# Performance work log

Hardware: AMD Instinct MI355X
Metric: run time of the kernel (lower is better)

## Reference

```python
import jax, jax.numpy as jnp
import numpy as np

NUM_HEADS = 8
LN_EPS = 1e-6


def _layer_norm(x, gamma, beta):
    mu = jnp.mean(x, axis=-1, keepdims=True)
    var = jnp.mean(jnp.square(x - mu), axis=-1, keepdims=True)
    return (x - mu) / jnp.sqrt(var + LN_EPS) * gamma + beta


def setup_inputs() -> dict:
    key = jax.random.key(0)
    B, S, H, F = 4, 2048, 1024, 4096
    ks = jax.random.split(key, 12)
    scale = 1.0 / np.sqrt(H)
    x = jax.random.normal(ks[0], (B, S, H), dtype=jnp.float32)
    # additive padding mask: 1 where masked, 0 where attended
    mask = jax.random.randint(ks[1], (B, 1, 1, S), 0, 2).astype(jnp.float32)
    Wq = jax.random.normal(ks[2], (H, H), dtype=jnp.float32) * scale
    Wk = jax.random.normal(ks[3], (H, H), dtype=jnp.float32) * scale
    Wv = jax.random.normal(ks[4], (H, H), dtype=jnp.float32) * scale
    Wo = jax.random.normal(ks[5], (H, H), dtype=jnp.float32) * scale
    W1 = jax.random.normal(ks[6], (H, F), dtype=jnp.float32) * scale
    b1 = jnp.zeros((F,), dtype=jnp.float32)
    W2 = jax.random.normal(ks[7], (F, H), dtype=jnp.float32) * (1.0 / np.sqrt(F))
    b2 = jnp.zeros((H,), dtype=jnp.float32)
    gamma = jnp.ones((H,), dtype=jnp.float32)
    beta = jnp.zeros((H,), dtype=jnp.float32)
    return {"x": x, "mask": mask, "Wq": Wq, "Wk": Wk, "Wv": Wv, "Wo": Wo,
            "W1": W1, "b1": b1, "W2": W2, "b2": b2, "gamma": gamma, "beta": beta}


def reference(x, mask, Wq, Wk, Wv, Wo, W1, b1, W2, b2, gamma, beta):
    B, S, H = x.shape
    nh = NUM_HEADS
    d = H // nh

    def split_heads(t):
        return t.reshape(B, S, nh, d).transpose(0, 2, 1, 3)  # [B,nh,S,d]

    q = split_heads(x @ Wq)
    k = split_heads(x @ Wk)
    v = split_heads(x @ Wv)

    # FAITHFUL to source bug: score /= d**(-0.5)  ==  score * sqrt(d)
    scores = jnp.einsum('bhqd,bhkd->bhqk', q, k) * jnp.sqrt(jnp.float32(d))
    scores = scores + mask * (-1e9)
    attn = jax.nn.softmax(scores, axis=-1)
    ctx = jnp.einsum('bhqk,bhkd->bhqd', attn, v)
    ctx = ctx.transpose(0, 2, 1, 3).reshape(B, S, H)
    attn_out = ctx @ Wo

    # dropout = identity (eval mode)
    x = _layer_norm(x + attn_out, gamma, beta)
    ffn = jnp.maximum(x @ W1 + b1, 0.0) @ W2 + b2
    x = _layer_norm(x + ffn, gamma, beta)
    return x
```

## Files before the change

### kernel.cpp

```cpp
#include <hip/hip_runtime.h>


typedef __bf16 bf16;
typedef __bf16 bf16x4 __attribute__((ext_vector_type(4)));
typedef __bf16 bf16x8 __attribute__((ext_vector_type(8)));
typedef float  f32x4  __attribute__((ext_vector_type(4)));

#define MFMA16(a, b, c) __builtin_amdgcn_mfma_f32_16x16x32_bf16(a, b, c, 0, 0, 0)

typedef const __attribute__((address_space(1))) void* gas_cptr;
typedef __attribute__((address_space(3))) void* las_ptr;

__device__ __forceinline__ void g2l16(const void* g, void* l) {
    __builtin_amdgcn_global_load_lds((gas_cptr)g, (las_ptr)l, 16, 0, 0);
}

__device__ __forceinline__ uint b16bits(bf16 v) {
    union { bf16 h; unsigned short u; } cv; cv.h = v; return (uint)cv.u;
}

__global__ __launch_bounds__(256) void split_f32_k(
    const float* __restrict__ in, bf16* __restrict__ hi, bf16* __restrict__ lo)
{
    const long i = (long)blockIdx.x * 256 + threadIdx.x;
    const float4 v = *(const float4*)(in + i * 4);
    const float a[4] = {v.x, v.y, v.z, v.w};
    bf16x4 h, l;
#pragma unroll
    for (int j = 0; j < 4; j++) {
        h[j] = (bf16)a[j];
        l[j] = (bf16)(a[j] - (float)h[j]);
    }
    *(bf16x4*)(hi + i * 4) = h;
    *(bf16x4*)(lo + i * 4) = l;
}

__global__ __launch_bounds__(256) void transpose_f32_k(
    const float* __restrict__ in, bf16* __restrict__ out_hi, bf16* __restrict__ out_lo,
    int in_rs, int out_rs)
{
    __shared__ uint Th[64][33];
    __shared__ uint Tl[64][33];
    const long c0 = (long)blockIdx.x * 64;
    const long r0 = (long)blockIdx.y * 64;
    const int t = threadIdx.x, rp = t >> 3, cc = t & 7;
    const float* pa = in + (r0 + 2 * rp) * (long)in_rs + c0 + cc * 8;
    const float* pb = pa + in_rs;
    float a[8], b[8];
    *(float4*)&a[0] = *(const float4*)pa;
    *(float4*)&a[4] = *(const float4*)(pa + 4);
    *(float4*)&b[0] = *(const float4*)pb;
    *(float4*)&b[4] = *(const float4*)(pb + 4);
#pragma unroll
    for (int j = 0; j < 8; j++) {
        const bf16 ah = (bf16)a[j], bh = (bf16)b[j];
        Th[cc * 8 + j][rp] = b16bits(ah) | (b16bits(bh) << 16);
        const bf16 al = (bf16)(a[j] - (float)ah), bl = (bf16)(b[j] - (float)bh);
        Tl[cc * 8 + j][rp] = b16bits(al) | (b16bits(bl) << 16);
    }
    __syncthreads();
#pragma unroll
    for (int i = 0; i < 2; i++) {
        const int task = i * 256 + t;
        const int c = task >> 3, ch = task & 7;
        uint4 wv;
        wv.x = Th[c][ch * 4 + 0]; wv.y = Th[c][ch * 4 + 1];
        wv.z = Th[c][ch * 4 + 2]; wv.w = Th[c][ch * 4 + 3];
        *(uint4*)(out_hi + (c0 + c) * (long)out_rs + r0 + ch * 8) = wv;
        if (out_lo) {
            uint4 wl;
            wl.x = Tl[c][ch * 4 + 0]; wl.y = Tl[c][ch * 4 + 1];
            wl.z = Tl[c][ch * 4 + 2]; wl.w = Tl[c][ch * 4 + 3];
            *(uint4*)(out_lo + (c0 + c) * (long)out_rs + r0 + ch * 8) = wl;
        }
    }
}

__global__ __launch_bounds__(256) void transpose_bf16_k(
    const bf16* __restrict__ in, bf16* __restrict__ out,
    int in_rs, int out_rs, int nh, long bo_in, long bi_in, long bo_out)
{
    __shared__ uint T[64][33];
    const int z = blockIdx.z;
    const bf16* inp = in + (long)(z / nh) * bo_in + (long)(z % nh) * bi_in;
    bf16* outp = out + (long)z * bo_out;
    const long c0 = (long)blockIdx.x * 64;
    const long r0 = (long)blockIdx.y * 64;
    const int t = threadIdx.x, rp = t >> 3, cc = t & 7;

    const uint4 ra = *(const uint4*)(inp + (r0 + 2 * rp) * (long)in_rs + c0 + cc * 8);
    const uint4 rb = *(const uint4*)(inp + (r0 + 2 * rp + 1) * (long)in_rs + c0 + cc * 8);
    const uint a32[4] = {ra.x, ra.y, ra.z, ra.w};
    const uint b32[4] = {rb.x, rb.y, rb.z, rb.w};
#pragma unroll
    for (int j = 0; j < 8; j++) {
        const uint av = (j & 1) ? (a32[j >> 1] >> 16) : (a32[j >> 1] & 0xffffu);
        const uint bv = (j & 1) ? (b32[j >> 1] >> 16) : (b32[j >> 1] & 0xffffu);
        T[cc * 8 + j][rp] = av | (bv << 16);
    }
    __syncthreads();
#pragma unroll
    for (int i = 0; i < 2; i++) {
        const int task = i * 256 + t;
        const int c = task >> 3, ch = task & 7;
        uint4 wv;
        wv.x = T[c][ch * 4 + 0]; wv.y = T[c][ch * 4 + 1];
        wv.z = T[c][ch * 4 + 2]; wv.w = T[c][ch * 4 + 3];
        *(uint4*)(outp + (c0 + c) * (long)out_rs + r0 + ch * 8) = wv;
    }
}

__global__ __launch_bounds__(256) void gemm_bf16_k(
    const bf16* __restrict__ A, const bf16* __restrict__ Bt,
    bf16* __restrict__ out,
    const float* __restrict__ bias, int relu, int M, int N, int K)
{
    __shared__ __align__(16) bf16 As[128 * 32];
    __shared__ __align__(16) bf16 Bs[128 * 32];
    const int t = threadIdx.x;
    const int fr = t & 15, fq = (t >> 4) & 3;
    const int w = t >> 6, wm = w & 1, wn = w >> 1;
    const long mBase = (long)blockIdx.y * 128;
    const long nBase = (long)blockIdx.x * 128;

    f32x4 acc[4][4];
#pragma unroll
    for (int i = 0; i < 4; i++)
#pragma unroll
        for (int j = 0; j < 4; j++) acc[i][j] = (f32x4){0.f, 0.f, 0.f, 0.f};

    const int arow = t >> 2;
    const int akc  = (t & 3) * 8;
    const bf16* ga0 = A + (mBase + arow) * (long)K + akc;
    const bf16* ga1 = A + (mBase + arow + 64) * (long)K + akc;
    const bf16* gb0 = Bt + (nBase + arow) * (long)K + akc;
    const bf16* gb1 = Bt + (nBase + arow + 64) * (long)K + akc;
    bf16* la0 = &As[t * 8];
    bf16* la1 = &As[(256 + t) * 8];
    bf16* lb0 = &Bs[t * 8];
    bf16* lb1 = &Bs[(256 + t) * 8];

    const int aoff = (wm * 64 + fr) * 32 + fq * 8;
    const int boff = (wn * 64 + fr) * 32 + fq * 8;

    for (int kt = 0; kt < K; kt += 32) {
        g2l16(ga0 + kt, la0);
        g2l16(ga1 + kt, la1);
        g2l16(gb0 + kt, lb0);
        g2l16(gb1 + kt, lb1);
        __syncthreads();
        bf16x8 af[4], bfv[4];
#pragma unroll
        for (int mt = 0; mt < 4; mt++) af[mt] = *(const bf16x8*)&As[aoff + mt * 512];
#pragma unroll
        for (int nt = 0; nt < 4; nt++) bfv[nt] = *(const bf16x8*)&Bs[boff + nt * 512];
#pragma unroll
        for (int mt = 0; mt < 4; mt++)
#pragma unroll
            for (int nt = 0; nt < 4; nt++)
                acc[mt][nt] = MFMA16(af[mt], bfv[nt], acc[mt][nt]);
        __syncthreads();
    }

    const long crow0 = mBase + wm * 64;
    const long ccol0 = nBase + wn * 64;
#pragma unroll
    for (int nt = 0; nt < 4; nt++) {
        const long col = ccol0 + nt * 16 + fr;
        const float bv = bias ? bias[col] : 0.0f;
#pragma unroll
        for (int mt = 0; mt < 4; mt++)
#pragma unroll
            for (int r = 0; r < 4; r++) {
                const long rowg = crow0 + mt * 16 + fq * 4 + r;
                float v = acc[mt][nt][r] + bv;
                if (relu) v = fmaxf(v, 0.0f);
                out[rowg * (long)N + col] = (bf16)v;
            }
    }
}

__global__ __launch_bounds__(256) void gemm_split_k(
    const bf16* __restrict__ Ah, const bf16* __restrict__ Al,
    const bf16* __restrict__ Bh, const bf16* __restrict__ Bl,
    bf16* __restrict__ out_hi, bf16* __restrict__ out_lo, int M, int N, int K)
{
    __shared__ __align__(16) bf16 Ahs[128 * 32];
    __shared__ __align__(16) bf16 Als[128 * 32];
    __shared__ __align__(16) bf16 Bhs[128 * 32];
    __shared__ __align__(16) bf16 Bls[128 * 32];
    const int t = threadIdx.x;
    const int fr = t & 15, fq = (t >> 4) & 3;
    const int w = t >> 6, wm = w & 1, wn = w >> 1;
    const long mBase = (long)blockIdx.y * 128;
    const long nBase = (long)blockIdx.x * 128;

    f32x4 acc[4][4];
#pragma unroll
    for (int i = 0; i < 4; i++)
#pragma unroll
        for (int j = 0; j < 4; j++) acc[i][j] = (f32x4){0.f, 0.f, 0.f, 0.f};

    const int arow = t >> 2;
    const int akc  = (t & 3) * 8;
    const long ga0 = (mBase + arow) * (long)K + akc;
    const long ga1 = (mBase + arow + 64) * (long)K + akc;
    const long gb0 = (nBase + arow) * (long)K + akc;
    const long gb1 = (nBase + arow + 64) * (long)K + akc;

    const int aoff = (wm * 64 + fr) * 32 + fq * 8;
    const int boff = (wn * 64 + fr) * 32 + fq * 8;

    for (int kt = 0; kt < K; kt += 32) {
        g2l16(Ah + ga0 + kt, &Ahs[t * 8]);
        g2l16(Ah + ga1 + kt, &Ahs[(256 + t) * 8]);
        g2l16(Al + ga0 + kt, &Als[t * 8]);
        g2l16(Al + ga1 + kt, &Als[(256 + t) * 8]);
        g2l16(Bh + gb0 + kt, &Bhs[t * 8]);
        g2l16(Bh + gb1 + kt, &Bhs[(256 + t) * 8]);
        g2l16(Bl + gb0 + kt, &Bls[t * 8]);
        g2l16(Bl + gb1 + kt, &Bls[(256 + t) * 8]);
        __syncthreads();
        bf16x8 ah[4], al[4], bh[4], bl[4];
#pragma unroll
        for (int mt = 0; mt < 4; mt++) {
            ah[mt] = *(const bf16x8*)&Ahs[aoff + mt * 512];
            al[mt] = *(const bf16x8*)&Als[aoff + mt * 512];
        }
#pragma unroll
        for (int nt = 0; nt < 4; nt++) {
            bh[nt] = *(const bf16x8*)&Bhs[boff + nt * 512];
            bl[nt] = *(const bf16x8*)&Bls[boff + nt * 512];
        }
#pragma unroll
        for (int mt = 0; mt < 4; mt++)
#pragma unroll
            for (int nt = 0; nt < 4; nt++) {
                acc[mt][nt] = MFMA16(ah[mt], bh[nt], acc[mt][nt]);
                acc[mt][nt] = MFMA16(ah[mt], bl[nt], acc[mt][nt]);
                acc[mt][nt] = MFMA16(al[mt], bh[nt], acc[mt][nt]);
            }
        __syncthreads();
    }

    const long crow0 = mBase + wm * 64;
    const long ccol0 = nBase + wn * 64;
#pragma unroll
    for (int nt = 0; nt < 4; nt++) {
        const long col = ccol0 + nt * 16 + fr;
#pragma unroll
        for (int mt = 0; mt < 4; mt++)
#pragma unroll
            for (int r = 0; r < 4; r++) {
                const long rowg = crow0 + mt * 16 + fq * 4 + r;
                const float v = acc[mt][nt][r];
                const long idx = rowg * (long)N + col;
                const bf16 h = (bf16)v;
                out_hi[idx] = h;
                out_lo[idx] = (bf16)(v - (float)h);
            }
    }
}

#define KROW 136
#define VROW 72
#define PROW 72
__global__ __launch_bounds__(256, 2) void flash_attn_k(
    const bf16* __restrict__ qhi, const bf16* __restrict__ qlo,
    const bf16* __restrict__ khi, const bf16* __restrict__ klo,
    const bf16* __restrict__ vt, const float* __restrict__ mask,
    bf16* __restrict__ ctx)
{
    __shared__ __align__(16) bf16 Kh[64 * KROW];
    __shared__ __align__(16) bf16 Kl[64 * KROW];
    __shared__ __align__(16) bf16 Vs[128 * VROW];
    __shared__ __align__(16) bf16 Ps[4][16 * PROW];
    const float scale = 11.3137085f;
    const int t = threadIdx.x, w = t >> 6;
    const int fr = t & 15, fq = (t >> 4) & 3;
    const int blk = blockIdx.x;
    const int qt = blk & 15, bh_ = blk >> 4, b = bh_ >> 3, h = bh_ & 7;
    const int qrow0 = qt * 128 + w * 16;

    bf16x8 qh[2][4], ql[2][4];
#pragma unroll
    for (int mt = 0; mt < 2; mt++) {
        const long qoff = ((long)(b * 2048 + qrow0 + mt * 64 + fr)) * 1024 + h * 128 + fq * 8;
#pragma unroll
        for (int s = 0; s < 4; s++) {
            qh[mt][s] = *(const bf16x8*)(qhi + qoff + s * 32);
            ql[mt][s] = *(const bf16x8*)(qlo + qoff + s * 32);
        }
    }
    f32x4 o[2][8];
#pragma unroll
    for (int mt = 0; mt < 2; mt++)
#pragma unroll
        for (int nt = 0; nt < 8; nt++) o[mt][nt] = (f32x4){0.f, 0.f, 0.f, 0.f};
    float m_run[2][4], l_run[2][4];
#pragma unroll
    for (int mt = 0; mt < 2; mt++)
#pragma unroll
        for (int r = 0; r < 4; r++) { m_run[mt][r] = -1e30f; l_run[mt][r] = 0.f; }

    const long kbase = (long)(b * 2048) * 1024 + h * 128 + (long)(t & 15) * 8;
    const long vbase = ((long)bh_ * 128) * 2048 + (long)(t & 7) * 8;
    const float* maskb = mask + b * 2048;

    for (int kt = 0; kt < 32; kt++) {
        __syncthreads();
#pragma unroll
        for (int i = 0; i < 4; i++) {
            const int key = i * 16 + (t >> 4);
            const long g = kbase + (long)(kt * 64 + key) * 1024;
            const bf16x8 vk_h = *(const bf16x8*)(khi + g);
            const bf16x8 vk_l = *(const bf16x8*)(klo + g);
            const int d = i * 32 + (t >> 3);
            const bf16x8 vv = *(const bf16x8*)(vt + vbase + (long)d * 2048 + kt * 64);
            *(bf16x8*)&Kh[key * KROW + (t & 15) * 8] = vk_h;
            *(bf16x8*)&Kl[key * KROW + (t & 15) * 8] = vk_l;
            *(bf16x8*)&Vs[d * VROW + (t & 7) * 8] = vv;
        }
        float madd[4];
#pragma unroll
        for (int ct = 0; ct < 4; ct++)
            madd[ct] = maskb[kt * 64 + ct * 16 + fr] * (-1e9f);
        __syncthreads();

        f32x4 sc[2][4];
#pragma unroll
        for (int mt = 0; mt < 2; mt++)
#pragma unroll
            for (int ct = 0; ct < 4; ct++) sc[mt][ct] = (f32x4){0.f, 0.f, 0.f, 0.f};
#pragma unroll
        for (int ct = 0; ct < 4; ct++)
#pragma unroll
            for (int s = 0; s < 4; s++) {
                const int off = (ct * 16 + fr) * KROW + s * 32 + fq * 8;
                const bf16x8 kh8 = *(const bf16x8*)&Kh[off];
                const bf16x8 kl8 = *(const bf16x8*)&Kl[off];
#pragma unroll
                for (int mt = 0; mt < 2; mt++) {
                    sc[mt][ct] = MFMA16(qh[mt][s], kh8, sc[mt][ct]);
                    sc[mt][ct] = MFMA16(qh[mt][s], kl8, sc[mt][ct]);
                    sc[mt][ct] = MFMA16(ql[mt][s], kh8, sc[mt][ct]);
                }
            }

#pragma unroll
        for (int mt = 0; mt < 2; mt++) {
            float alpha[4];
#pragma unroll
            for (int r = 0; r < 4; r++) {
                float mx = sc[mt][0][r] * scale + madd[0];
                mx = fmaxf(mx, sc[mt][1][r] * scale + madd[1]);
                mx = fmaxf(mx, sc[mt][2][r] * scale + madd[2]);
                mx = fmaxf(mx, sc[mt][3][r] * scale + madd[3]);
                mx = fmaxf(mx, __shfl_xor(mx, 1));
                mx = fmaxf(mx, __shfl_xor(mx, 2));
                mx = fmaxf(mx, __shfl_xor(mx, 4));
                mx = fmaxf(mx, __shfl_xor(mx, 8));
                const float mn = fmaxf(m_run[mt][r], mx);
                alpha[r] = __expf(m_run[mt][r] - mn);
                m_run[mt][r] = mn;
            }
            float lt[4] = {0.f, 0.f, 0.f, 0.f};
#pragma unroll
            for (int ct = 0; ct < 4; ct++)
#pragma unroll
                for (int r = 0; r < 4; r++) {
                    const float p = __expf(sc[mt][ct][r] * scale + madd[ct] - m_run[mt][r]);
                    lt[r] += p;
                    Ps[w][(fq * 4 + r) * PROW + ct * 16 + fr] = (bf16)p;
                }
#pragma unroll
            for (int r = 0; r < 4; r++) {
                float s_ = lt[r];
                s_ += __shfl_xor(s_, 1); s_ += __shfl_xor(s_, 2);
                s_ += __shfl_xor(s_, 4); s_ += __shfl_xor(s_, 8);
                l_run[mt][r] = l_run[mt][r] * alpha[r] + s_;
            }
#pragma unroll
            for (int nt = 0; nt < 8; nt++)
#pragma unroll
                for (int r = 0; r < 4; r++) o[mt][nt][r] *= alpha[r];

#pragma unroll
            for (int sp = 0; sp < 2; sp++) {
                const bf16x8 pf = *(const bf16x8*)&Ps[w][fr * PROW + sp * 32 + fq * 8];
#pragma unroll
                for (int nt = 0; nt < 8; nt++) {
                    const bf16x8 vf = *(const bf16x8*)&Vs[(nt * 16 + fr) * VROW + sp * 32 + fq * 8];
                    o[mt][nt] = MFMA16(pf, vf, o[mt][nt]);
                }
            }
        }
    }
#pragma unroll
    for (int mt = 0; mt < 2; mt++)
#pragma unroll
        for (int r = 0; r < 4; r++) {
            const float inv = l_run[mt][r] > 0.f ? 1.0f / l_run[mt][r] : 0.f;
#pragma unroll
            for (int nt = 0; nt < 8; nt++) {
                const long idx = ((long)(b * 2048 + qrow0 + mt * 64 + fq * 4 + r)) * 1024
                               + h * 128 + nt * 16 + fr;
                ctx[idx] = (bf16)(o[mt][nt][r] * inv);
            }
        }
}

__global__ __launch_bounds__(256) void add_ln_k(
    const float* __restrict__ xf, const bf16* __restrict__ y,
    const float* __restrict__ gamma, const float* __restrict__ beta,
    float* __restrict__ out, bf16* __restrict__ out_b)
{
    __shared__ float red[8];
    const long row = blockIdx.x;
    const int t = threadIdx.x, lane = t & 63, w = t >> 6;
    float v[4];
    const float4 xv = *(const float4*)(xf + row * 1024 + t * 4);
    v[0] = xv.x; v[1] = xv.y; v[2] = xv.z; v[3] = xv.w;
    const bf16x4 yv = *(const bf16x4*)(y + row * 1024 + t * 4);
    float s = 0.f, s2 = 0.f;
#pragma unroll
    for (int i = 0; i < 4; i++) {
        v[i] += (float)yv[i];
        s += v[i]; s2 += v[i] * v[i];
    }
#pragma unroll
    for (int off = 1; off < 64; off <<= 1) {
        s += __shfl_xor(s, off);
        s2 += __shfl_xor(s2, off);
    }
    if (lane == 0) { red[w] = s; red[4 + w] = s2; }
    __syncthreads();
    s = red[0] + red[1] + red[2] + red[3];
    s2 = red[4] + red[5] + red[6] + red[7];
    const float mean = s * (1.0f / 1024.0f);
    const float var = s2 * (1.0f / 1024.0f) - mean * mean;
    const float rstd = rsqrtf(var + 1e-6f);
    float4 ov;
    ov.x = (v[0] - mean) * rstd * gamma[t * 4 + 0] + beta[t * 4 + 0];
    ov.y = (v[1] - mean) * rstd * gamma[t * 4 + 1] + beta[t * 4 + 1];
    ov.z = (v[2] - mean) * rstd * gamma[t * 4 + 2] + beta[t * 4 + 2];
    ov.w = (v[3] - mean) * rstd * gamma[t * 4 + 3] + beta[t * 4 + 3];
    *(float4*)(out + row * 1024 + t * 4) = ov;
    if (out_b) {
        bf16x4 hb;
        hb[0] = (bf16)ov.x; hb[1] = (bf16)ov.y; hb[2] = (bf16)ov.z; hb[3] = (bf16)ov.w;
        *(bf16x4*)(out_b + row * 1024 + t * 4) = hb;
    }
}

extern "C" void kernel_launch(void* const* d_in, const int* in_sizes, int n_in,
                              void* d_out, int out_size, void* d_ws, size_t ws_size,
                              hipStream_t stream)
{
    (void)in_sizes; (void)n_in; (void)out_size; (void)ws_size;
    const float* x     = (const float*)d_in[0];
    const float* mask  = (const float*)d_in[1];
    const float* Wq    = (const float*)d_in[2];
    const float* Wk    = (const float*)d_in[3];
    const float* Wv    = (const float*)d_in[4];
    const float* Wo    = (const float*)d_in[5];
    const float* W1    = (const float*)d_in[6];
    const float* b1    = (const float*)d_in[7];
    const float* W2    = (const float*)d_in[8];
    const float* b2    = (const float*)d_in[9];
    const float* gamma = (const float*)d_in[10];
    const float* beta  = (const float*)d_in[11];
    float* out = (float*)d_out;

    char* ws = (char*)d_ws;
    const size_t SZ = 8192ul * 1024 * 2;
    bf16* qhi  = (bf16*)(ws + 0 * SZ);
    bf16* qlo  = (bf16*)(ws + 1 * SZ);
    bf16* khi  = (bf16*)(ws + 2 * SZ);
    bf16* klo  = (bf16*)(ws + 3 * SZ);
    bf16* hbuf = (bf16*)(ws + 0 * SZ);
    bf16* vbuf = (bf16*)(ws + 4 * SZ);
    bf16* ctxb = vbuf;
    bf16* vtb  = (bf16*)(ws + 5 * SZ);
    bf16* fbuf = vtb;
    bf16* xh   = (bf16*)(ws + 6 * SZ);
    bf16* xl   = (bf16*)(ws + 7 * SZ);
    bf16* aob  = xl;
    float* x1f = (float*)(ws + 8 * SZ);
    bf16* x1b  = (bf16*)(ws + 10 * SZ);
    char* wts  = ws + 11 * SZ;
    bf16* Wqth = (bf16*)(wts);
    bf16* Wqtl = (bf16*)(wts + 1 * 2097152);
    bf16* Wkth = (bf16*)(wts + 2 * 2097152);
    bf16* Wktl = (bf16*)(wts + 3 * 2097152);
    bf16* Wvt  = (bf16*)(wts + 4 * 2097152);
    bf16* Wot  = (bf16*)(wts + 5 * 2097152);
    bf16* W1t  = (bf16*)(wts + 6 * 2097152);
    bf16* W2t  = (bf16*)(wts + 6 * 2097152 + 8388608);

    const dim3 blk(256);
    split_f32_k<<<dim3(8192), blk, 0, stream>>>(x, xh, xl);
    transpose_f32_k<<<dim3(16, 16), blk, 0, stream>>>(Wq, Wqth, Wqtl, 1024, 1024);
    transpose_f32_k<<<dim3(16, 16), blk, 0, stream>>>(Wk, Wkth, Wktl, 1024, 1024);
    transpose_f32_k<<<dim3(16, 16), blk, 0, stream>>>(Wv, Wvt, nullptr, 1024, 1024);
    transpose_f32_k<<<dim3(16, 16), blk, 0, stream>>>(Wo, Wot, nullptr, 1024, 1024);
    transpose_f32_k<<<dim3(64, 16), blk, 0, stream>>>(W1, W1t, nullptr, 4096, 1024);
    transpose_f32_k<<<dim3(16, 64), blk, 0, stream>>>(W2, W2t, nullptr, 1024, 4096);
    gemm_split_k<<<dim3(8, 64), blk, 0, stream>>>(xh, xl, Wqth, Wqtl, qhi, qlo, 8192, 1024, 1024);
    gemm_split_k<<<dim3(8, 64), blk, 0, stream>>>(xh, xl, Wkth, Wktl, khi, klo, 8192, 1024, 1024);
    gemm_bf16_k<<<dim3(8, 64), blk, 0, stream>>>(xh, Wvt, vbuf, nullptr, 0, 8192, 1024, 1024);
    transpose_bf16_k<<<dim3(2, 32, 32), blk, 0, stream>>>(vbuf, vtb, 1024, 2048, 8,
                                                          (long)2048 * 1024, 128L, (long)128 * 2048);
    flash_attn_k<<<dim3(512), blk, 0, stream>>>(qhi, qlo, khi, klo, vtb, mask, ctxb);
    gemm_bf16_k<<<dim3(8, 64), blk, 0, stream>>>(ctxb, Wot, aob, nullptr, 0, 8192, 1024, 1024);
    add_ln_k<<<dim3(8192), blk, 0, stream>>>(x, aob, gamma, beta, x1f, x1b);
    gemm_bf16_k<<<dim3(32, 64), blk, 0, stream>>>(x1b, W1t, hbuf, b1, 1, 8192, 4096, 1024);
    gemm_bf16_k<<<dim3(8, 64), blk, 0, stream>>>(hbuf, W2t, fbuf, b2, 0, 8192, 1024, 4096);
    add_ln_k<<<dim3(8192), blk, 0, stream>>>(x1f, fbuf, gamma, beta, out, nullptr);
}
```

Measured before the change: 745.5 us.

## Use 8 waves per flash-attention block with one 16-row tile each

The flash attention kernel now launches 512 threads per block, and each of the 8 waves owns a single 16-row query tile instead of two. This halves per-thread register state and should allow more waves per CU while sharing the same K/V tile. It also wraps the MFMA sections in s_setprio and skips rescaling the output accumulator when no row maximum changed. The risks are heavier barrier synchronisation across more waves and fewer key/value loads per thread to hide latency.

```diff
diff --git a/kernel.cpp b/kernel.cpp
--- a/kernel.cpp
+++ b/kernel.cpp
@@ -265,7 +265,7 @@
 #define KROW 136
 #define VROW 72
 #define PROW 72
-__global__ __launch_bounds__(256, 2) void flash_attn_k(
+__global__ __launch_bounds__(512, 4) void flash_attn_k(
     const bf16* __restrict__ qhi, const bf16* __restrict__ qlo,
     const bf16* __restrict__ khi, const bf16* __restrict__ klo,
     const bf16* __restrict__ vt, const float* __restrict__ mask,
@@ -274,7 +274,7 @@
     __shared__ __align__(16) bf16 Kh[64 * KROW];
     __shared__ __align__(16) bf16 Kl[64 * KROW];
     __shared__ __align__(16) bf16 Vs[128 * VROW];
-    __shared__ __align__(16) bf16 Ps[4][16 * PROW];
+    __shared__ __align__(16) bf16 Ps[8][16 * PROW];
     const float scale = 11.3137085f;
     const int t = threadIdx.x, w = t >> 6;
     const int fr = t & 15, fq = (t >> 4) & 3;
@@ -282,26 +282,21 @@
     const int qt = blk & 15, bh_ = blk >> 4, b = bh_ >> 3, h = bh_ & 7;
     const int qrow0 = qt * 128 + w * 16;
 
-    bf16x8 qh[2][4], ql[2][4];
-#pragma unroll
-    for (int mt = 0; mt < 2; mt++) {
-        const long qoff = ((long)(b * 2048 + qrow0 + mt * 64 + fr)) * 1024 + h * 128 + fq * 8;
+    bf16x8 qh[4], ql[4];
+    {
+        const long qoff = ((long)(b * 2048 + qrow0 + fr)) * 1024 + h * 128 + fq * 8;
 #pragma unroll
         for (int s = 0; s < 4; s++) {
-            qh[mt][s] = *(const bf16x8*)(qhi + qoff + s * 32);
-            ql[mt][s] = *(const bf16x8*)(qlo + qoff + s * 32);
-        }
-    }
-    f32x4 o[2][8];
-#pragma unroll
-    for (int mt = 0; mt < 2; mt++)
-#pragma unroll
-        for (int nt = 0; nt < 8; nt++) o[mt][nt] = (f32x4){0.f, 0.f, 0.f, 0.f};
-    float m_run[2][4], l_run[2][4];
-#pragma unroll
-    for (int mt = 0; mt < 2; mt++)
-#pragma unroll
-        for (int r = 0; r < 4; r++) { m_run[mt][r] = -1e30f; l_run[mt][r] = 0.f; }
+            qh[s] = *(const bf16x8*)(qhi + qoff + s * 32);
+            ql[s] = *(const bf16x8*)(qlo + qoff + s * 32);
+        }
+    }
+    f32x4 o[8];
+#pragma unroll
+    for (int nt = 0; nt < 8; nt++) o[nt] = (f32x4){0.f, 0.f, 0.f, 0.f};
+    float m_run[4], l_run[4];
+#pragma unroll
+    for (int r = 0; r < 4; r++) { m_run[r] = -1e30f; l_run[r] = 0.f; }
 
     const long kbase = (long)(b * 2048) * 1024 + h * 128 + (long)(t & 15) * 8;
     const long vbase = ((long)bh_ * 128) * 2048 + (long)(t & 7) * 8;
@@ -310,12 +305,12 @@
     for (int kt = 0; kt < 32; kt++) {
         __syncthreads();
 #pragma unroll
-        for (int i = 0; i < 4; i++) {
-            const int key = i * 16 + (t >> 4);
+        for (int i = 0; i < 2; i++) {
+            const int key = i * 32 + (t >> 4);
             const long g = kbase + (long)(kt * 64 + key) * 1024;
             const bf16x8 vk_h = *(const bf16x8*)(khi + g);
             const bf16x8 vk_l = *(const bf16x8*)(klo + g);
-            const int d = i * 32 + (t >> 3);
+            const int d = i * 64 + (t >> 3);
             const bf16x8 vv = *(const bf16x8*)(vt + vbase + (long)d * 2048 + kt * 64);
             *(bf16x8*)&Kh[key * KROW + (t & 15) * 8] = vk_h;
             *(bf16x8*)&Kl[key * KROW + (t & 15) * 8] = vk_l;
@@ -327,87 +322,85 @@
             madd[ct] = maskb[kt * 64 + ct * 16 + fr] * (-1e9f);
         __syncthreads();
 
-        f32x4 sc[2][4];
-#pragma unroll
-        for (int mt = 0; mt < 2; mt++)
-#pragma unroll
-            for (int ct = 0; ct < 4; ct++) sc[mt][ct] = (f32x4){0.f, 0.f, 0.f, 0.f};
-#pragma unroll
-        for (int ct = 0; ct < 4; ct++)
-#pragma unroll
-            for (int s = 0; s < 4; s++) {
+        f32x4 sc[4];
+#pragma unroll
+        for (int ct = 0; ct < 4; ct++) sc[ct] = (f32x4){0.f, 0.f, 0.f, 0.f};
+        __builtin_amdgcn_s_setprio(1);
+#pragma unroll
+        for (int s = 0; s < 4; s++)
+#pragma unroll
+            for (int ct = 0; ct < 4; ct++) {
                 const int off = (ct * 16 + fr) * KROW + s * 32 + fq * 8;
                 const bf16x8 kh8 = *(const bf16x8*)&Kh[off];
                 const bf16x8 kl8 = *(const bf16x8*)&Kl[off];
-#pragma unroll
-                for (int mt = 0; mt < 2; mt++) {
-                    sc[mt][ct] = MFMA16(qh[mt][s], kh8, sc[mt][ct]);
-                    sc[mt][ct] = MFMA16(qh[mt][s], kl8, sc[mt][ct]);
-                    sc[mt][ct] = MFMA16(ql[mt][s], kh8, sc[mt][ct]);
-                }
+                sc[ct] = MFMA16(qh[s], kh8, sc[ct]);
+                sc[ct] = MFMA16(qh[s], kl8, sc[ct]);
+                sc[ct] = MFMA16(ql[s], kh8, sc[ct]);
             }
-
-#pragma unroll
-        for (int mt = 0; mt < 2; mt++) {
-            float alpha[4];
+        __builtin_amdgcn_s_setprio(0);
+
+        float alpha[4];
+#pragma unroll
+        for (int r = 0; r < 4; r++) {
+            float mx = sc[0][r] * scale + madd[0];
+            mx = fmaxf(mx, sc[1][r] * scale + madd[1]);
+            mx = fmaxf(mx, sc[2][r] * scale + madd[2]);
+            mx = fmaxf(mx, sc[3][r] * scale + madd[3]);
+            mx = fmaxf(mx, __shfl_xor(mx, 1));
+            mx = fmaxf(mx, __shfl_xor(mx, 2));
+            mx = fmaxf(mx, __shfl_xor(mx, 4));
+            mx = fmaxf(mx, __shfl_xor(mx, 8));
+            const float mn = fmaxf(m_run[r], mx);
+            alpha[r] = __expf(m_run[r] - mn);
+            m_run[r] = mn;
+        }
+        float lt[4] = {0.f, 0.f, 0.f, 0.f};
+#pragma unroll
+        for (int ct = 0; ct < 4; ct++)
 #pragma unroll
             for (int r = 0; r < 4; r++) {
-                float mx = sc[mt][0][r] * scale + madd[0];
-                mx = fmaxf(mx, sc[mt][1][r] * scale + madd[1]);
-                mx = fmaxf(mx, sc[mt][2][r] * scale + madd[2]);
-                mx = fmaxf(mx, sc[mt][3][r] * scale + madd[3]);
-                mx = fmaxf(mx, __shfl_xor(mx, 1));
-                mx = fmaxf(mx, __shfl_xor(mx, 2));
-                mx = fmaxf(mx, __shfl_xor(mx, 4));
-                mx = fmaxf(mx, __shfl_xor(mx, 8));
-                const float mn = fmaxf(m_run[mt][r], mx);
-                alpha[r] = __expf(m_run[mt][r] - mn);
-                m_run[mt][r] = mn;
+                const float p = __expf(sc[ct][r] * scale + madd[ct] - m_run[r]);
+                lt[r] += p;
+                Ps[w][(fq * 4 + r) * PROW + ct * 16 + fr] = (bf16)p;
             }
-            float lt[4] = {0.f, 0.f, 0.f, 0.f};
-#pragma unroll
-            for (int ct = 0; ct < 4; ct++)
-#pragma unroll
-                for (int r = 0; r < 4; r++) {
-                    const float p = __expf(sc[mt][ct][r] * scale + madd[ct] - m_run[mt][r]);
-                    lt[r] += p;
-                    Ps[w][(fq * 4 + r) * PROW + ct * 16 + fr] = (bf16)p;
-                }
-#pragma unroll
-            for (int r = 0; r < 4; r++) {
-                float s_ = lt[r];
-                s_ += __shfl_xor(s_, 1); s_ += __shfl_xor(s_, 2);
-                s_ += __shfl_xor(s_, 4); s_ += __shfl_xor(s_, 8);
-                l_run[mt][r] = l_run[mt][r] * alpha[r] + s_;
+#pragma unroll
+        for (int r = 0; r < 4; r++) {
+            float s_ = lt[r];
+            s_ += __shfl_xor(s_, 1); s_ += __shfl_xor(s_, 2);
+            s_ += __shfl_xor(s_, 4); s_ += __shfl_xor(s_, 8);
+            l_run[r] = l_run[r] * alpha[r] + s_;
+        }
+        const int need = (alpha[0] < 1.f) | (alpha[1] < 1.f) |
+                         (alpha[2] < 1.f) | (alpha[3] < 1.f);
+        if (__any(need)) {
+#pragma unroll
+            for (int nt = 0; nt < 8; nt++)
+#pragma unroll
+                for (int r = 0; r < 4; r++) o[nt][r] *= alpha[r];
+        }
+
+        __builtin_amdgcn_s_setprio(1);
+#pragma unroll
+        for (int sp = 0; sp < 2; sp++) {
+            const bf16x8 pf = *(const bf16x8*)&Ps[w][fr * PROW + sp * 32 + fq * 8];
+#pragma unroll
+            for (int nt = 0; nt < 8; nt++) {
+                const bf16x8 vf = *(const bf16x8*)&Vs[(nt * 16 + fr) * VROW + sp * 32 + fq * 8];
+                o[nt] = MFMA16(pf, vf, o[nt]);
             }
-#pragma unroll
-            for (int nt = 0; nt < 8; nt++)
-#pragma unroll
-                for (int r = 0; r < 4; r++) o[mt][nt][r] *= alpha[r];
-
-#pragma unroll
-            for (int sp = 0; sp < 2; sp++) {
-                const bf16x8 pf = *(const bf16x8*)&Ps[w][fr * PROW + sp * 32 + fq * 8];
-#pragma unroll
-                for (int nt = 0; nt < 8; nt++) {
-                    const bf16x8 vf = *(const bf16x8*)&Vs[(nt * 16 + fr) * VROW + sp * 32 + fq * 8];
-                    o[mt][nt] = MFMA16(pf, vf, o[mt][nt]);
-                }
-            }
-        }
-    }
-#pragma unroll
-    for (int mt = 0; mt < 2; mt++)
-#pragma unroll
-        for (int r = 0; r < 4; r++) {
-            const float inv = l_run[mt][r] > 0.f ? 1.0f / l_run[mt][r] : 0.f;
-#pragma unroll
-            for (int nt = 0; nt < 8; nt++) {
-                const long idx = ((long)(b * 2048 + qrow0 + mt * 64 + fq * 4 + r)) * 1024
-                               + h * 128 + nt * 16 + fr;
-                ctx[idx] = (bf16)(o[mt][nt][r] * inv);
-            }
-        }
+        }
+        __builtin_amdgcn_s_setprio(0);
+    }
+#pragma unroll
+    for (int r = 0; r < 4; r++) {
+        const float inv = l_run[r] > 0.f ? 1.0f / l_run[r] : 0.f;
+#pragma unroll
+        for (int nt = 0; nt < 8; nt++) {
+            const long idx = ((long)(b * 2048 + qrow0 + fq * 4 + r)) * 1024
+                           + h * 128 + nt * 16 + fr;
+            ctx[idx] = (bf16)(o[nt][r] * inv);
+        }
+    }
 }
 
 __global__ __launch_bounds__(256) void add_ln_k(
@@ -511,7 +504,7 @@
     gemm_bf16_k<<<dim3(8, 64), blk, 0, stream>>>(xh, Wvt, vbuf, nullptr, 0, 8192, 1024, 1024);
     transpose_bf16_k<<<dim3(2, 32, 32), blk, 0, stream>>>(vbuf, vtb, 1024, 2048, 8,
                                                           (long)2048 * 1024, 128L, (long)128 * 2048);
-    flash_attn_k<<<dim3(512), blk, 0, stream>>>(qhi, qlo, khi, klo, vtb, mask, ctxb);
+    flash_attn_k<<<dim3(512), dim3(512), 0, stream>>>(qhi, qlo, khi, klo, vtb, mask, ctxb);
     gemm_bf16_k<<<dim3(8, 64), blk, 0, stream>>>(ctxb, Wot, aob, nullptr, 0, 8192, 1024, 1024);
     add_ln_k<<<dim3(8192), blk, 0, stream>>>(x, aob, gamma, beta, x1f, x1b);
     gemm_bf16_k<<<dim3(32, 64), blk, 0, stream>>>(x1b, W1t, hbuf, b1, 1, 8192, 4096, 1024);
```

Measured after the change: 812.1 us. 1.09x slower.
